# Performance work log

Hardware: AMD Instinct MI355X
Metric: run time of the kernel (lower is better)

The kernel has to match this reference:

```python
import jax, jax.numpy as jnp
import numpy as np

EPS = 1e-5

def _ln(x, g, b):
    m = jnp.mean(x, axis=-1, keepdims=True)
    v = jnp.var(x, axis=-1, keepdims=True)
    return (x - m) / jnp.sqrt(v + EPS) * g + b

def setup_inputs() -> dict:
    key = jax.random.key(0)
    ks = jax.random.split(key, 16)
    B, T, N, K, d, E = 2, 12, 512, 8, 64, 64
    D = K * d
    s = 0.02
    inp = {
        "x": jax.random.normal(ks[0], (B, T, N, D), jnp.float32),
        "lapmatrix": jax.random.normal(ks[1], (N, N), jnp.float32),
        "node_embeddings": jax.random.normal(ks[2], (N, E), jnp.float32),
        "Wq": jax.random.normal(ks[3], (D, D), jnp.float32) * s,
        "bq": jnp.zeros((D,), jnp.float32),
        "Wk": jax.random.normal(ks[4], (D, D), jnp.float32) * s,
        "bk": jnp.zeros((D,), jnp.float32),
        "Wv": jax.random.normal(ks[5], (D, D), jnp.float32) * s,
        "bv": jnp.zeros((D,), jnp.float32),
        "Wo": jax.random.normal(ks[6], (D, D), jnp.float32) * s,
        "bo": jnp.zeros((D,), jnp.float32),
        "W1": jax.random.normal(ks[7], (4 * D, D), jnp.float32) * s,
        "b1": jnp.zeros((4 * D,), jnp.float32),
        "W2": jax.random.normal(ks[8], (D, 4 * D), jnp.float32) * s,
        "b2": jnp.zeros((D,), jnp.float32),
        "g1": jnp.ones((D,), jnp.float32),
        "be1": jnp.zeros((D,), jnp.float32),
        "g2": jnp.ones((D,), jnp.float32),
        "be2": jnp.zeros((D,), jnp.float32),
        "alpha": jnp.float32(1.0),
        "beta": jnp.float32(1.0),
        "k": 3,
    }
    return inp

def reference(x, lapmatrix, node_embeddings, Wq, bq, Wk, bk, Wv, bv, Wo, bo,
              W1, b1, W2, b2, g1, be1, g2, be2, alpha, beta, k):
    B, T, N, D = x.shape
    K, d = 8, D // 8
    x_raw = x
    xn = _ln(x, g1, be1)
    q = (xn @ Wq.T + bq).reshape(B, T, N, K, d)
    kk = (xn @ Wk.T + bk).reshape(B, T, N, K, d)
    v = (xn @ Wv.T + bv).reshape(B, T, N, K, d)
    # raw attention logits: [B,T,K,N,N]
    raw = jnp.einsum('btnkd,btmkd->btknm', q, kk) / jnp.sqrt(jnp.float32(d))
    # graph biases, all [N,N], broadcast over B,T,K
    supports = jax.nn.softmax(jax.nn.relu(node_embeddings @ node_embeddings.T), axis=1)
    adj = (lapmatrix != 0).astype(x.dtype)
    mask = jnp.where(adj == 0, jnp.float32(-1e9), jnp.float32(0.0))
    logits = raw + alpha * supports + beta * lapmatrix + mask
    attn = jax.nn.softmax(logits, axis=-1)  # dropout = identity in eval
    out = jnp.einsum('btknm,btmkd->btnkd', attn, v).reshape(B, T, N, D)
    x1 = x_raw + (out @ Wo.T + bo)
    h = _ln(x1, g2, be2)
    ffn = jax.nn.relu(h @ W1.T + b1) @ W2.T + b2
    return x1 + ffn
```

## Files before the change

### kernel.cpp

```cpp
#include <hip/hip_runtime.h>

typedef unsigned short u16;
typedef unsigned int   u32;
typedef __attribute__((ext_vector_type(8))) short bf16x8;
typedef __attribute__((ext_vector_type(4))) float f32x4;

#define DEV static __device__ __forceinline__

DEV float b2f(u16 u){ return __uint_as_float(((u32)u)<<16); }
DEV u16 f2b(float f){
  u32 u = __float_as_uint(f);
  u32 r = (u + 0x7FFFu + ((u>>16)&1u)) >> 16;
  return (u16)r;
}

union V8 { uint4 v; u16 s[8]; };

DEV u32 cvt_pk_bf16(float lo, float hi){
  u32 r;
  asm("v_cvt_pk_bf16_f32 %0, %1, %2" : "=v"(r) : "v"(lo), "v"(hi));
  return r;
}

DEV bool is_f32(const void* dt){ return *(const u32*)dt == 0x3F800000u; }

DEV uint4 ld8_ext_bf(const void* p, size_t i, bool f32){
  if(f32){
    const float* q = (const float*)p + i;
    float4 a = *(const float4*)q, b = *(const float4*)(q+4);
    V8 r;
    r.s[0]=f2b(a.x); r.s[1]=f2b(a.y); r.s[2]=f2b(a.z); r.s[3]=f2b(a.w);
    r.s[4]=f2b(b.x); r.s[5]=f2b(b.y); r.s[6]=f2b(b.z); r.s[7]=f2b(b.w);
    return r.v;
  }
  return *(const uint4*)((const u16*)p + i);
}
DEV void ld8_ext_f(const void* p, size_t i, bool f32, float* o){
  if(f32){
    const float* q = (const float*)p + i;
    float4 a = *(const float4*)q, b = *(const float4*)(q+4);
    o[0]=a.x;o[1]=a.y;o[2]=a.z;o[3]=a.w;o[4]=b.x;o[5]=b.y;o[6]=b.z;o[7]=b.w;
  }else{
    V8 u; u.v = *(const uint4*)((const u16*)p + i);
    #pragma unroll
    for(int k=0;k<8;k++) o[k]=b2f(u.s[k]);
  }
}
DEV float ld1_ext(const void* p, size_t i, bool f32){
  return f32 ? ((const float*)p)[i] : b2f(((const u16*)p)[i]);
}
DEV float load_scalar(const void* p, bool f32){
  return f32 ? *(const float*)p : b2f(*(const u16*)p);
}

DEV void gl_lds16(const u16* g, u16* l){
  __builtin_amdgcn_global_load_lds((const __attribute__((address_space(1))) void*)g,
                                   (__attribute__((address_space(3))) void*)l, 16, 0, 0);
}

__global__ __launch_bounds__(256) void sentinel_kernel(u16* out, long n, const void* dt){
  long ne = is_f32(dt) ? 2*n : n;
  long i = (long)blockIdx.x*256 + threadIdx.x;
  if(i < ne) out[i] = 0x4442;
}

__global__ __launch_bounds__(256) void convert_w_kernel(
    const void* Wq, const void* Wk, const void* Wv, const void* Wo,
    const void* W1, const void* W2, u16* __restrict__ wbf, const void* dt)
{
  const bool f32 = is_f32(dt);
  size_t i = ((size_t)blockIdx.x*256 + threadIdx.x)*8;
  const void* src; size_t base;
  if(i < 262144){ src=Wq; base=0; }
  else if(i < 524288){ src=Wk; base=262144; }
  else if(i < 786432){ src=Wv; base=524288; }
  else if(i < 1048576){ src=Wo; base=786432; }
  else if(i < 2097152){ src=W1; base=1048576; }
  else { src=W2; base=2097152; }
  *(uint4*)(wbf + i) = ld8_ext_bf(src, i-base, f32);
}

__global__ __launch_bounds__(256) void convert_b_kernel(
    const void* bq, const void* bk, const void* bv, const void* bo,
    const void* b1, const void* b2, float* __restrict__ bfp, const void* dt)
{
  const bool f32 = is_f32(dt);
  int j = blockIdx.x*256 + threadIdx.x;
  if(j >= 4608) return;
  const void* src; int off;
  if(j < 512){ src=bq; off=0; }
  else if(j < 1024){ src=bk; off=512; }
  else if(j < 1536){ src=bv; off=1024; }
  else if(j < 2048){ src=bo; off=1536; }
  else if(j < 4096){ src=b1; off=2048; }
  else { src=b2; off=4096; }
  bfp[j] = ld1_ext(src, j-off, f32);
}

__global__ __launch_bounds__(256) void bias_kernel(
    const void* __restrict__ E, const void* __restrict__ lap,
    const void* __restrict__ alpha_p, const void* __restrict__ beta_p,
    float* __restrict__ bm, const void* dt)
{
  __shared__ u16 Et[64*520];
  __shared__ float red[8];
  const bool f32 = is_f32(dt);
  const int t = threadIdx.x, n = blockIdx.x;
  for(int i=0;i<16;i++){
    int c = t + i*256;
    int m = c >> 3, j0 = (c & 7) * 8;
    V8 u; u.v = ld8_ext_bf(E, (size_t)m*64 + j0, f32);
    #pragma unroll
    for(int jj=0;jj<8;jj++) Et[(j0+jj)*520 + m] = u.s[jj];
  }
  __syncthreads();
  const float alpha = load_scalar(alpha_p, f32);
  const float beta  = load_scalar(beta_p, f32);
  float sc0=0.f, sc1=0.f;
  const int m0 = t, m1 = t+256;
  for(int kk=0;kk<64;kk++){
    float en = b2f(Et[kk*520+n]);
    sc0 += en * b2f(Et[kk*520+m0]);
    sc1 += en * b2f(Et[kk*520+m1]);
  }
  sc0 = fmaxf(sc0, 0.f); sc1 = fmaxf(sc1, 0.f);
  float mx = fmaxf(sc0, sc1);
  for(int o=1;o<64;o<<=1) mx = fmaxf(mx, __shfl_xor(mx,o,64));
  const int wave = t>>6;
  if((t&63)==0) red[wave]=mx;
  __syncthreads();
  mx = fmaxf(fmaxf(red[0],red[1]), fmaxf(red[2],red[3]));
  float e0 = __expf(sc0-mx), e1 = __expf(sc1-mx);
  float sm = e0+e1;
  for(int o=1;o<64;o<<=1) sm += __shfl_xor(sm,o,64);
  if((t&63)==0) red[4+wave]=sm;
  __syncthreads();
  sm = red[4]+red[5]+red[6]+red[7];
  const float inv = 1.f/sm;
  float lv0 = ld1_ext(lap, (size_t)n*512+m0, f32);
  bm[n*512+m0] = alpha*e0*inv + beta*lv0 + (lv0==0.f ? -1e9f : 0.f);
  float lv1 = ld1_ext(lap, (size_t)n*512+m1, f32);
  bm[n*512+m1] = alpha*e1*inv + beta*lv1 + (lv1==0.f ? -1e9f : 0.f);
}

template<int EXTIN>
__global__ __launch_bounds__(64) void ln_kernel(const void* __restrict__ xin,
    const void* __restrict__ g, const void* __restrict__ b, u16* __restrict__ out,
    const void* dt)
{
  const bool f32 = is_f32(dt);
  const int row = blockIdx.x, lane = threadIdx.x;
  float v[8];
  if(EXTIN){
    ld8_ext_f(xin, (size_t)row*512 + lane*8, f32, v);
  }else{
    V8 u; u.v = *(const uint4*)((const u16*)xin + (size_t)row*512 + lane*8);
    #pragma unroll
    for(int i=0;i<8;i++) v[i]=b2f(u.s[i]);
  }
  float s=0.f, ss=0.f;
  #pragma unroll
  for(int i=0;i<8;i++){ s+=v[i]; ss+=v[i]*v[i]; }
  #pragma unroll
  for(int o=1;o<64;o<<=1){ s+=__shfl_xor(s,o,64); ss+=__shfl_xor(ss,o,64); }
  const float mean = s*(1.0f/512.0f);
  const float var  = ss*(1.0f/512.0f) - mean*mean;
  const float rstd = rsqrtf(var + 1e-5f);
  float gv[8], bv[8];
  ld8_ext_f(g, (size_t)lane*8, f32, gv);
  ld8_ext_f(b, (size_t)lane*8, f32, bv);
  V8 o8;
  #pragma unroll
  for(int i=0;i<8;i++) o8.s[i]=f2b((v[i]-mean)*rstd*gv[i]+bv[i]);
  *(uint4*)(out+(size_t)row*512+lane*8)=o8.v;
}

template<int RELU, int RES, int RESEXT, int OUTEXT>
__global__ __launch_bounds__(256) void gemm_nt(
    const u16* __restrict__ A, const u16* __restrict__ B,
    const float* __restrict__ bias, const void* __restrict__ resid,
    void* __restrict__ Cout, int N, int K, const void* dt)
{
  __shared__ u16 As[128*64];
  __shared__ u16 Bs[128*64];
  const bool f32 = is_f32(dt);
  const int t = threadIdx.x;
  const int wave = t>>6, lane = t&63;
  const int n0 = blockIdx.y*128, m0 = blockIdx.x*128;
  const int wr = wave>>1, wc = wave&1;

  f32x4 acc[4][4];
  #pragma unroll
  for(int i=0;i<4;i++)
    #pragma unroll
    for(int j=0;j<4;j++){ acc[i][j][0]=0.f; acc[i][j][1]=0.f; acc[i][j][2]=0.f; acc[i][j][3]=0.f; }

  const int lrow8 = lane>>3, lg = lane&7;
  const int gsw = (lg ^ lrow8)*8;
  const u16* Ag = A + (size_t)(m0+lrow8)*K + gsw;
  const u16* Bg = B + (size_t)(n0+lrow8)*K + gsw;
  const int fr = lane&15, qd = lane>>4, frk = (fr&7);

  for(int k0=0; k0<K; k0+=64){
    __syncthreads();
    #pragma unroll
    for(int i=0;i<4;i++){
      int c = wave*4+i;
      gl_lds16(Ag + (size_t)(c*8)*K + k0, &As[c*512]);
      gl_lds16(Bg + (size_t)(c*8)*K + k0, &Bs[c*512]);
    }
    __syncthreads();
    #pragma unroll
    for(int s=0;s<2;s++){
      const int slot = ((s*4+qd) ^ frk)*8;
      bf16x8 af[4], bfr[4];
      #pragma unroll
      for(int i=0;i<4;i++) af[i] = *(const bf16x8*)&As[(wr*64+i*16+fr)*64 + slot];
      #pragma unroll
      for(int j=0;j<4;j++) bfr[j] = *(const bf16x8*)&Bs[(wc*64+j*16+fr)*64 + slot];
      #pragma unroll
      for(int i=0;i<4;i++)
        #pragma unroll
        for(int j=0;j<4;j++)
          acc[i][j] = __builtin_amdgcn_mfma_f32_16x16x32_bf16(af[i], bfr[j], acc[i][j], 0,0,0);
    }
  }

  const int col16 = lane&15, rbase = (lane>>4)*4;
  #pragma unroll
  for(int i=0;i<4;i++){
    #pragma unroll
    for(int j=0;j<4;j++){
      const int gc = n0 + wc*64 + j*16 + col16;
      const float bv = bias[gc];
      #pragma unroll
      for(int r=0;r<4;r++){
        const int gr = m0 + wr*64 + i*16 + rbase + r;
        float val = acc[i][j][r] + bv;
        if(RELU) val = fmaxf(val, 0.f);
        if(RES){
          if(RESEXT) val += ld1_ext(resid, (size_t)gr*N+gc, f32);
          else       val += b2f(((const u16*)resid)[(size_t)gr*N+gc]);
        }
        if(OUTEXT && f32) ((float*)Cout)[(size_t)gr*N+gc] = val;
        else              ((u16*)Cout)[(size_t)gr*N+gc] = f2b(val);
      }
    }
  }
}

template<int RELU, int RES, int RESEXT, int OUTEXT>
__global__ __launch_bounds__(256) void gemm_nt64(
    const u16* __restrict__ A, const u16* __restrict__ B,
    const float* __restrict__ bias, const void* __restrict__ resid,
    void* __restrict__ Cout, int N, int K, const void* dt)
{
  __shared__ u16 As[128*64];
  __shared__ u16 Bs[64*64];
  const bool f32 = is_f32(dt);
  const int t = threadIdx.x;
  const int wave = t>>6, lane = t&63;
  const int n0 = blockIdx.y*64, m0 = blockIdx.x*128;
  const int wr = wave>>1, wc = wave&1;

  f32x4 acc[4][2];
  #pragma unroll
  for(int i=0;i<4;i++)
    #pragma unroll
    for(int j=0;j<2;j++){ acc[i][j][0]=0.f; acc[i][j][1]=0.f; acc[i][j][2]=0.f; acc[i][j][3]=0.f; }

  const int lrow8 = lane>>3, lg = lane&7;
  const int gsw = (lg ^ lrow8)*8;
  const u16* Ag = A + (size_t)(m0+lrow8)*K + gsw;
  const u16* Bg = B + (size_t)(n0+lrow8)*K + gsw;
  const int fr = lane&15, qd = lane>>4, frk = (fr&7);

  for(int k0=0; k0<K; k0+=64){
    __syncthreads();
    #pragma unroll
    for(int i=0;i<4;i++){
      int c = wave*4+i;
      gl_lds16(Ag + (size_t)(c*8)*K + k0, &As[c*512]);
    }
    #pragma unroll
    for(int i=0;i<2;i++){
      int c = wave*2+i;
      gl_lds16(Bg + (size_t)(c*8)*K + k0, &Bs[c*512]);
    }
    __syncthreads();
    #pragma unroll
    for(int s=0;s<2;s++){
      const int slot = ((s*4+qd) ^ frk)*8;
      bf16x8 af[4], bfr[2];
      #pragma unroll
      for(int i=0;i<4;i++) af[i] = *(const bf16x8*)&As[(wr*64+i*16+fr)*64 + slot];
      #pragma unroll
      for(int j=0;j<2;j++) bfr[j] = *(const bf16x8*)&Bs[(wc*32+j*16+fr)*64 + slot];
      #pragma unroll
      for(int i=0;i<4;i++)
        #pragma unroll
        for(int j=0;j<2;j++)
          acc[i][j] = __builtin_amdgcn_mfma_f32_16x16x32_bf16(af[i], bfr[j], acc[i][j], 0,0,0);
    }
  }

  const int col16 = lane&15, rbase = (lane>>4)*4;
  #pragma unroll
  for(int i=0;i<4;i++){
    #pragma unroll
    for(int j=0;j<2;j++){
      const int gc = n0 + wc*32 + j*16 + col16;
      const float bv = bias[gc];
      #pragma unroll
      for(int r=0;r<4;r++){
        const int gr = m0 + wr*64 + i*16 + rbase + r;
        float val = acc[i][j][r] + bv;
        if(RELU) val = fmaxf(val, 0.f);
        if(RES){
          if(RESEXT) val += ld1_ext(resid, (size_t)gr*N+gc, f32);
          else       val += b2f(((const u16*)resid)[(size_t)gr*N+gc]);
        }
        if(OUTEXT && f32) ((float*)Cout)[(size_t)gr*N+gc] = val;
        else              ((u16*)Cout)[(size_t)gr*N+gc] = f2b(val);
      }
    }
  }
}

__global__ __launch_bounds__(256,3) void attn_kernel(
    const u16* __restrict__ qkv, const float* __restrict__ bm,
    u16* __restrict__ out)
{
  __shared__ u16 Vt[2][64*136];

  const int QS = 1536;
  const int t = threadIdx.x, wave = t>>6, lane = t&63;
  const int head = blockIdx.y, bt = blockIdx.z;
  const int q0 = blockIdx.x*128 + wave*32;
  const u16* qp = qkv + (size_t)bt*512*QS + head*64;
  const u16* kp = qp + 512;
  const u16* vp = qp + 1024;

  const int l16 = lane&15, qd = lane>>4;

  const int srow = t>>1, shalf = (t&1)*32;
  const u16* vcp = vp + (size_t)srow*QS + shalf;

  uint4 vv[4];
  #pragma unroll
  for(int qi=0;qi<4;qi++) vv[qi] = *(const uint4*)(vcp + qi*8);

  bf16x8 qf[2][2];
  #pragma unroll
  for(int i=0;i<2;i++)
    #pragma unroll
    for(int kc=0;kc<2;kc++)
      qf[i][kc] = *(const bf16x8*)(qp + (size_t)(q0 + i*16 + l16)*QS + kc*32 + qd*8);

  const float* bmr0 = bm + (size_t)(q0 + l16)*512;
  const float* bmr1 = bmr0 + 16*512;

  const int arow = ((l16>>2)<<3) + (l16&3);
  const u16* kfb = kp + (size_t)arow*QS + qd*8;

  float mrun[2], lrun[2];
  mrun[0] = -3e38f; mrun[1] = -3e38f;
  lrun[0] = 0.f;    lrun[1] = 0.f;
  f32x4 oacc[2][4];
  #pragma unroll
  for(int i=0;i<2;i++)
    #pragma unroll
    for(int j=0;j<4;j++){ oacc[i][j][0]=0.f; oacc[i][j][1]=0.f; oacc[i][j][2]=0.f; oacc[i][j][3]=0.f; }

  #pragma unroll
  for(int qi=0;qi<4;qi++){
    V8 u; u.v = vv[qi];
    #pragma unroll
    for(int jj=0;jj<8;jj++) Vt[0][(shalf + qi*8 + jj)*136 + srow] = u.s[jj];
  }
  __syncthreads();

  #pragma unroll
  for(int c=0;c<4;c++){
    bf16x8 kfA[4][2], kfB[4][2];
    #pragma unroll
    for(int tt=0;tt<4;tt++){
      const u16* kr = kfb + (size_t)(c*128 + tt*32)*QS;
      kfA[tt][0] = *(const bf16x8*)(kr);
      kfA[tt][1] = *(const bf16x8*)(kr + 32);
    }
    #pragma unroll
    for(int tt=0;tt<4;tt++){
      const u16* kr = kfb + (size_t)(c*128 + tt*32 + 4)*QS;
      kfB[tt][0] = *(const bf16x8*)(kr);
      kfB[tt][1] = *(const bf16x8*)(kr + 32);
    }
    uint4 vvn[4];
    if(c<3){
      #pragma unroll
      for(int qi=0;qi<4;qi++) vvn[qi] = *(const uint4*)(vcp + (size_t)((c+1)*128)*QS + qi*8);
    }

    f32x4 p[2][8];
    __builtin_amdgcn_s_setprio(1);
    #pragma unroll
    for(int tt=0;tt<4;tt++){
      #pragma unroll
      for(int i=0;i<2;i++){
        f32x4 s; s[0]=0.f; s[1]=0.f; s[2]=0.f; s[3]=0.f;
        s = __builtin_amdgcn_mfma_f32_16x16x32_bf16(kfA[tt][0], qf[i][0], s, 0,0,0);
        s = __builtin_amdgcn_mfma_f32_16x16x32_bf16(kfA[tt][1], qf[i][1], s, 0,0,0);
        p[i][tt] = s;
      }
    }
    #pragma unroll
    for(int tt=0;tt<4;tt++){
      #pragma unroll
      for(int i=0;i<2;i++){
        f32x4 s; s[0]=0.f; s[1]=0.f; s[2]=0.f; s[3]=0.f;
        s = __builtin_amdgcn_mfma_f32_16x16x32_bf16(kfB[tt][0], qf[i][0], s, 0,0,0);
        s = __builtin_amdgcn_mfma_f32_16x16x32_bf16(kfB[tt][1], qf[i][1], s, 0,0,0);
        p[i][tt+4] = s;
      }
    }
    __builtin_amdgcn_s_setprio(0);

    #pragma unroll
    for(int i=0;i<2;i++){
      const float* br = (i ? bmr1 : bmr0) + c*128 + qd*8;
      float mx = -3e38f;
      #pragma unroll
      for(int tt=0;tt<8;tt++){
        const float4 b4 = *(const float4*)(br + (tt&3)*32 + ((tt>>2)<<2));
        p[i][tt][0] = p[i][tt][0]*0.125f + b4.x;
        p[i][tt][1] = p[i][tt][1]*0.125f + b4.y;
        p[i][tt][2] = p[i][tt][2]*0.125f + b4.z;
        p[i][tt][3] = p[i][tt][3]*0.125f + b4.w;
        mx = fmaxf(mx, fmaxf(fmaxf(p[i][tt][0],p[i][tt][1]), fmaxf(p[i][tt][2],p[i][tt][3])));
      }
      mx = fmaxf(mx, __shfl_xor(mx, 16, 64));
      mx = fmaxf(mx, __shfl_xor(mx, 32, 64));
      const float mnew = fmaxf(mrun[i], mx);
      if(__any(mx > mrun[i])){
        const float al = __expf(mrun[i] - mnew);
        lrun[i] *= al;
        #pragma unroll
        for(int r=0;r<4;r++){
          const float alr = __shfl(al, (qd<<2)+r, 64);
          #pragma unroll
          for(int j=0;j<4;j++) oacc[i][j][r] *= alr;
        }
      }
      mrun[i] = mnew;
      float rs = 0.f;
      #pragma unroll
      for(int tt=0;tt<8;tt++){
        p[i][tt][0] = __expf(p[i][tt][0]-mnew);
        p[i][tt][1] = __expf(p[i][tt][1]-mnew);
        p[i][tt][2] = __expf(p[i][tt][2]-mnew);
        p[i][tt][3] = __expf(p[i][tt][3]-mnew);
        rs += (p[i][tt][0]+p[i][tt][1]) + (p[i][tt][2]+p[i][tt][3]);
      }
      rs += __shfl_xor(rs, 16, 64);
      rs += __shfl_xor(rs, 32, 64);
      lrun[i] += rs;
    }

    __builtin_amdgcn_s_setprio(1);
    #pragma unroll
    for(int ks=0;ks<4;ks++){
      union { bf16x8 v; u32 w[4]; } pa[2];
      #pragma unroll
      for(int i=0;i<2;i++){
        pa[i].w[0] = cvt_pk_bf16(p[i][ks][0],   p[i][ks][1]);
        pa[i].w[1] = cvt_pk_bf16(p[i][ks][2],   p[i][ks][3]);
        pa[i].w[2] = cvt_pk_bf16(p[i][ks+4][0], p[i][ks+4][1]);
        pa[i].w[3] = cvt_pk_bf16(p[i][ks+4][2], p[i][ks+4][3]);
      }
      #pragma unroll
      for(int j=0;j<4;j++){
        bf16x8 bvf = *(const bf16x8*)&Vt[c&1][(j*16 + l16)*136 + ks*32 + qd*8];
        oacc[0][j] = __builtin_amdgcn_mfma_f32_16x16x32_bf16(pa[0].v, bvf, oacc[0][j], 0,0,0);
        oacc[1][j] = __builtin_amdgcn_mfma_f32_16x16x32_bf16(pa[1].v, bvf, oacc[1][j], 0,0,0);
      }
    }
    __builtin_amdgcn_s_setprio(0);

    if(c<3){
      #pragma unroll
      for(int qi=0;qi<4;qi++){
        V8 u; u.v = vvn[qi];
        #pragma unroll
        for(int jj=0;jj<8;jj++) Vt[(c+1)&1][(shalf + qi*8 + jj)*136 + srow] = u.s[jj];
      }
      __syncthreads();
    }
  }

  u16* op = out + (size_t)bt*512*512 + head*64;
  #pragma unroll
  for(int i=0;i<2;i++){
    const float inv = 1.f / lrun[i];
    #pragma unroll
    for(int r=0;r<4;r++){
      const float invr = __shfl(inv, (qd<<2)+r, 64);
      const size_t rowb = (size_t)(q0 + i*16 + qd*4 + r)*512;
      #pragma unroll
      for(int j=0;j<4;j++)
        op[rowb + j*16 + l16] = f2b(oacc[i][j][r] * invr);
    }
  }
}

extern "C" void kernel_launch(void* const* d_in, const int* in_sizes, int n_in,
                              void* d_out, int out_size, void* d_ws, size_t ws_size,
                              hipStream_t stream) {
  const void* x   = d_in[0];
  const void* lap = d_in[1];
  const void* ne  = d_in[2];
  const void* Wq  = d_in[3];
  const void* bq  = d_in[4];
  const void* Wk  = d_in[5];
  const void* bk  = d_in[6];
  const void* Wv  = d_in[7];
  const void* bv  = d_in[8];
  const void* Wo  = d_in[9];
  const void* bo  = d_in[10];
  const void* W1  = d_in[11];
  const void* b1  = d_in[12];
  const void* W2  = d_in[13];
  const void* b2  = d_in[14];
  const void* g1  = d_in[15];
  const void* be1 = d_in[16];
  const void* g2  = d_in[17];
  const void* be2 = d_in[18];
  const void* alpha = d_in[19];
  const void* beta  = d_in[20];
  const void* dt = g1;

  const int M = 12288;
  const size_t NEED = (size_t)512*512*4 + (size_t)M*512*2*2 + (size_t)M*2048*2
                    + (size_t)3145728*2 + (size_t)4608*4;
  if(ws_size < NEED){
    long n = out_size;
    sentinel_kernel<<<(2*n+255)/256, 256, 0, stream>>>((u16*)d_out, n, dt);
    return;
  }
  char* w = (char*)d_ws;
  float* bias_m = (float*)w;              w += (size_t)512*512*4;
  u16*   slotB  = (u16*)w;                w += (size_t)M*512*2;
  char*  slotC  = w;                      w += (size_t)M*2048*2;
  u16*   x1     = (u16*)w;                w += (size_t)M*512*2;
  u16*   wbf    = (u16*)w;                w += (size_t)3145728*2;
  float* bfp    = (float*)w;
  u16* qkv = (u16*)slotC;
  u16* h1  = (u16*)slotC;
  u16* xn = slotB;
  u16* ao = slotB;
  u16* h  = slotB;

  convert_w_kernel<<<1536, 256, 0, stream>>>(Wq, Wk, Wv, Wo, W1, W2, wbf, dt);
  convert_b_kernel<<<18, 256, 0, stream>>>(bq, bk, bv, bo, b1, b2, bfp, dt);
  bias_kernel<<<512, 256, 0, stream>>>(ne, lap, alpha, beta, bias_m, dt);
  ln_kernel<1><<<M, 64, 0, stream>>>(x, g1, be1, xn, dt);
  gemm_nt<0,0,0,0><<<dim3(96,12), 256, 0, stream>>>(xn, wbf, bfp, nullptr, qkv, 1536, 512, dt);
  attn_kernel<<<dim3(4,8,24), 256, 0, stream>>>(qkv, bias_m, ao);
  gemm_nt64<0,1,1,0><<<dim3(96,8), 256, 0, stream>>>(ao, wbf+786432, bfp+1536, x, x1, 512, 512, dt);
  ln_kernel<0><<<M, 64, 0, stream>>>(x1, g2, be2, h, dt);
  gemm_nt<1,0,0,0><<<dim3(96,16), 256, 0, stream>>>(h, wbf+1048576, bfp+2048, nullptr, h1, 2048, 512, dt);
  gemm_nt64<0,1,0,1><<<dim3(96,8), 256, 0, stream>>>(h1, wbf+2097152, bfp+4096, x1, d_out, 512, 2048, dt);
}
```

Measured before the change: 337.5 us.

## Stage K tiles in swizzled LDS and pre-permute bias matrix for coalesced loads

K chunks are now loaded into a swizzled shared-memory buffer via direct global-to-LDS copies and prefetched for the next chunk, instead of each wave reading K fragments from global memory into registers. The bias matrix producer writes in a permuted layout matching the MFMA fragment order, so the attention kernel can read it with contiguous float4 loads. This aims to cut redundant global K traffic across waves and uncoalesced bias reads, at the cost of extra LDS use (possibly lower occupancy) and an added barrier per chunk.

After: 330.8 us. 1.02x faster.

```diff
diff --git a/kernel.cpp b/kernel.cpp
--- a/kernel.cpp
+++ b/kernel.cpp
@@ -137,10 +137,20 @@
   __syncthreads();
   sm = red[4]+red[5]+red[6]+red[7];
   const float inv = 1.f/sm;
+  const int q0b = n>>5, iq = (n>>4)&1, l16 = n&15;
+  const size_t qpart = (size_t)q0b*256 + (size_t)l16*4 + iq;
   float lv0 = ld1_ext(lap, (size_t)n*512+m0, f32);
-  bm[n*512+m0] = alpha*e0*inv + beta*lv0 + (lv0==0.f ? -1e9f : 0.f);
+  {
+    float val = alpha*e0*inv + beta*lv0 + (lv0==0.f ? -1e9f : 0.f);
+    int kb = m0>>3, e = m0&7;
+    bm[(size_t)kb*4096 + qpart + (e>>1)*64 + (e&1)*2] = val;
+  }
   float lv1 = ld1_ext(lap, (size_t)n*512+m1, f32);
-  bm[n*512+m1] = alpha*e1*inv + beta*lv1 + (lv1==0.f ? -1e9f : 0.f);
+  {
+    float val = alpha*e1*inv + beta*lv1 + (lv1==0.f ? -1e9f : 0.f);
+    int kb = m1>>3, e = m1&7;
+    bm[(size_t)kb*4096 + qpart + (e>>1)*64 + (e&1)*2] = val;
+  }
 }
 
 template<int EXTIN>
@@ -331,6 +341,7 @@
     const u16* __restrict__ qkv, const float* __restrict__ bm,
     u16* __restrict__ out)
 {
+  __shared__ u16 Kb[128*64];
   __shared__ u16 Vt[2][64*136];
 
   const int QS = 1536;
@@ -343,9 +354,16 @@
 
   const int l16 = lane&15, qd = lane>>4;
 
+  const int lrow8 = lane>>3, lg = lane&7;
   const int srow = t>>1, shalf = (t&1)*32;
   const u16* vcp = vp + (size_t)srow*QS + shalf;
 
+  #pragma unroll
+  for(int ii=0;ii<4;ii++){
+    const int c8 = wave*4 + ii;
+    const int pg = lg ^ ((2*(lrow8&3) + (c8&3)) & 7);
+    gl_lds16(kp + (size_t)(c8*8 + lrow8)*QS + pg*8, &Kb[c8*512]);
+  }
   uint4 vv[4];
   #pragma unroll
   for(int qi=0;qi<4;qi++) vv[qi] = *(const uint4*)(vcp + qi*8);
@@ -357,11 +375,13 @@
     for(int kc=0;kc<2;kc++)
       qf[i][kc] = *(const bf16x8*)(qp + (size_t)(q0 + i*16 + l16)*QS + kc*32 + qd*8);
 
-  const float* bmr0 = bm + (size_t)(q0 + l16)*512;
-  const float* bmr1 = bmr0 + 16*512;
+  const float* bml = bm + (size_t)(blockIdx.x*4 + wave)*256 + (size_t)qd*4096 + (size_t)l16*4;
 
   const int arow = ((l16>>2)<<3) + (l16&3);
-  const u16* kfb = kp + (size_t)arow*QS + qd*8;
+  const int rperm = (2*(l16&3) + (l16>>2)) & 7;
+  const int g0 = (qd ^ rperm)*8;
+  const u16* KA0 = &Kb[arow*64 + g0];
+  const u16* KA1 = &Kb[arow*64 + (g0 ^ 32)];
 
   float mrun[2], lrun[2];
   mrun[0] = -3e38f; mrun[1] = -3e38f;
@@ -382,62 +402,63 @@
 
   #pragma unroll
   for(int c=0;c<4;c++){
-    bf16x8 kfA[4][2], kfB[4][2];
-    #pragma unroll
-    for(int tt=0;tt<4;tt++){
-      const u16* kr = kfb + (size_t)(c*128 + tt*32)*QS;
-      kfA[tt][0] = *(const bf16x8*)(kr);
-      kfA[tt][1] = *(const bf16x8*)(kr + 32);
-    }
-    #pragma unroll
-    for(int tt=0;tt<4;tt++){
-      const u16* kr = kfb + (size_t)(c*128 + tt*32 + 4)*QS;
-      kfB[tt][0] = *(const bf16x8*)(kr);
-      kfB[tt][1] = *(const bf16x8*)(kr + 32);
-    }
-    uint4 vvn[4];
-    if(c<3){
-      #pragma unroll
-      for(int qi=0;qi<4;qi++) vvn[qi] = *(const uint4*)(vcp + (size_t)((c+1)*128)*QS + qi*8);
-    }
-
     f32x4 p[2][8];
     __builtin_amdgcn_s_setprio(1);
     #pragma unroll
-    for(int tt=0;tt<4;tt++){
+    for(int tt=0;tt<8;tt++){
+      const int ro = (tt&3)*2048 + (tt>>2)*256;
+      bf16x8 a0 = *(const bf16x8*)(KA0 + ro);
+      bf16x8 a1 = *(const bf16x8*)(KA1 + ro);
       #pragma unroll
       for(int i=0;i<2;i++){
         f32x4 s; s[0]=0.f; s[1]=0.f; s[2]=0.f; s[3]=0.f;
-        s = __builtin_amdgcn_mfma_f32_16x16x32_bf16(kfA[tt][0], qf[i][0], s, 0,0,0);
-        s = __builtin_amdgcn_mfma_f32_16x16x32_bf16(kfA[tt][1], qf[i][1], s, 0,0,0);
+        s = __builtin_amdgcn_mfma_f32_16x16x32_bf16(a0, qf[i][0], s, 0,0,0);
+        s = __builtin_amdgcn_mfma_f32_16x16x32_bf16(a1, qf[i][1], s, 0,0,0);
         p[i][tt] = s;
       }
     }
-    #pragma unroll
-    for(int tt=0;tt<4;tt++){
+    __builtin_amdgcn_s_setprio(0);
+    if(c<3){
+      __syncthreads();
+      #pragma unroll
+      for(int ii=0;ii<4;ii++){
+        const int c8 = wave*4 + ii;
+        const int pg = lg ^ ((2*(lrow8&3) + (c8&3)) & 7);
+        gl_lds16(kp + (size_t)((c+1)*128 + c8*8 + lrow8)*QS + pg*8, &Kb[c8*512]);
+      }
+      #pragma unroll
+      for(int qi=0;qi<4;qi++) vv[qi] = *(const uint4*)(vcp + (size_t)((c+1)*128)*QS + qi*8);
+    }
+
+    float mx0 = -3e38f, mx1 = -3e38f;
+    #pragma unroll
+    for(int s4=0;s4<4;s4++){
+      const float* bp = bml + c*65536 + s4*16384;
+      const float4 bg0 = *(const float4*)(bp);
+      const float4 bg1 = *(const float4*)(bp + 64);
+      const float4 bg2 = *(const float4*)(bp + 128);
+      const float4 bg3 = *(const float4*)(bp + 192);
       #pragma unroll
       for(int i=0;i<2;i++){
-        f32x4 s; s[0]=0.f; s[1]=0.f; s[2]=0.f; s[3]=0.f;
-        s = __builtin_amdgcn_mfma_f32_16x16x32_bf16(kfB[tt][0], qf[i][0], s, 0,0,0);
-        s = __builtin_amdgcn_mfma_f32_16x16x32_bf16(kfB[tt][1], qf[i][1], s, 0,0,0);
-        p[i][tt+4] = s;
-      }
-    }
-    __builtin_amdgcn_s_setprio(0);
+        f32x4& pl = p[i][s4];
+        pl[0] = pl[0]*0.125f + (i ? bg0.y : bg0.x);
+        pl[1] = pl[1]*0.125f + (i ? bg0.w : bg0.z);
+        pl[2] = pl[2]*0.125f + (i ? bg1.y : bg1.x);
+        pl[3] = pl[3]*0.125f + (i ? bg1.w : bg1.z);
+        f32x4& ph = p[i][s4+4];
+        ph[0] = ph[0]*0.125f + (i ? bg2.y : bg2.x);
+        ph[1] = ph[1]*0.125f + (i ? bg2.w : bg2.z);
+        ph[2] = ph[2]*0.125f + (i ? bg3.y : bg3.x);
+        ph[3] = ph[3]*0.125f + (i ? bg3.w : bg3.z);
+        const float m8 = fmaxf(fmaxf(fmaxf(pl[0],pl[1]),fmaxf(pl[2],pl[3])),
+                               fmaxf(fmaxf(ph[0],ph[1]),fmaxf(ph[2],ph[3])));
+        if(i==0) mx0 = fmaxf(mx0, m8); else mx1 = fmaxf(mx1, m8);
+      }
+    }
 
     #pragma unroll
     for(int i=0;i<2;i++){
-      const float* br = (i ? bmr1 : bmr0) + c*128 + qd*8;
-      float mx = -3e38f;
-      #pragma unroll
-      for(int tt=0;tt<8;tt++){
-        const float4 b4 = *(const float4*)(br + (tt&3)*32 + ((tt>>2)<<2));
-        p[i][tt][0] = p[i][tt][0]*0.125f + b4.x;
-        p[i][tt][1] = p[i][tt][1]*0.125f + b4.y;
-        p[i][tt][2] = p[i][tt][2]*0.125f + b4.z;
-        p[i][tt][3] = p[i][tt][3]*0.125f + b4.w;
-        mx = fmaxf(mx, fmaxf(fmaxf(p[i][tt][0],p[i][tt][1]), fmaxf(p[i][tt][2],p[i][tt][3])));
-      }
+      float mx = i ? mx1 : mx0;
       mx = fmaxf(mx, __shfl_xor(mx, 16, 64));
       mx = fmaxf(mx, __shfl_xor(mx, 32, 64));
       const float mnew = fmaxf(mrun[i], mx);
@@ -489,7 +510,7 @@
     if(c<3){
       #pragma unroll
       for(int qi=0;qi<4;qi++){
-        V8 u; u.v = vvn[qi];
+        V8 u; u.v = vv[qi];
         #pragma unroll
         for(int jj=0;jj<8;jj++) Vt[(c+1)&1][(shalf + qi*8 + jj)*136 + srow] = u.s[jj];
       }
```
